# Kernel tuning notes

Measured on AMD Instinct MI355X. Metric: run time of the kernel, lower is better.

Reference implementation:

```python
import jax, jax.numpy as jnp
import numpy as np

B, L, H = 4, 96, 512
R, T = 257, 21


def setup_inputs() -> dict:
    key = jax.random.key(0)
    ks = jax.random.split(key, 7)
    std_in = (2.0 / (H + 1 + R)) ** 0.5  # xavier_normal over [H+1, R]
    return {
        "layer1": jax.random.normal(ks[0], (B, L, H), jnp.float32),
        "layer2": jax.random.normal(ks[1], (B, L, H), jnp.float32),
        "layer3": jax.random.normal(ks[2], (B, L, H), jnp.float32),
        "W_1": jax.random.normal(ks[3], (H + 1, R), jnp.float32) * std_in,
        "W_2": jax.random.normal(ks[4], (H + 1, R), jnp.float32) * std_in,
        "W_3": jax.random.normal(ks[5], (H + 1, R), jnp.float32) * std_in,
        "W_l": jax.random.normal(ks[6], (1, R, T), jnp.float32),
    }


def reference(layer1, layer2, layer3, W_1, W_2, W_3, W_l):
    # Append bias-ones feature, as in the torch forward.
    ones = jnp.ones((*layer1.shape[:2], 1), layer1.dtype)
    l1 = jnp.concatenate([layer1, ones], axis=-1)  # [n, i, H+1]
    l2 = jnp.concatenate([layer2, ones], axis=-1)  # [n, j, H+1]
    l3 = jnp.concatenate([layer3, jnp.ones((*layer3.shape[:-1], 1), layer3.dtype)], axis=-1)
    # Factor the CP contraction: project each stream to rank space first.
    p1 = jnp.einsum("nia,ar->nir", l1, W_1)  # [n, i, r]
    p2 = jnp.einsum("njb,br->njr", l2, W_2)  # [n, j, r]
    p3 = jnp.einsum("nkc,cr->nkr", l3, W_3)  # [n, k, r]
    # Fold label map into one stream, then rank-reduce outer product.
    p3t = jnp.einsum("nkr,rt->ntkr", p3, W_l[0])  # [n, t, k, r]
    out = jnp.einsum("nir,njr,ntkr->ntijk", p1, p2, p3t)  # [n, t, i, j, k]
    return out
```

## Files before the change

kernel.cpp:

```cpp
#include <hip/hip_runtime.h>
#include <hip/hip_bf16.h>

#define RR 257
#define RP 288
#define TT 21

typedef __attribute__((ext_vector_type(4))) float f32x4;
typedef __attribute__((ext_vector_type(8))) short bf16x8;

union Pack8 { unsigned short s[8]; uint4 v; };

__device__ __forceinline__ unsigned short f2b(float f) {
    union { float f; unsigned u; } v; v.f = f;
    unsigned r = v.u + 0x7fffu + ((v.u >> 16) & 1u);
    return (unsigned short)(r >> 16);
}

__global__ __launch_bounds__(384) void proj_kernel(
    const float* __restrict__ l1, const float* __restrict__ l2, const float* __restrict__ l3,
    const float* __restrict__ W1, const float* __restrict__ W2, const float* __restrict__ W3,
    float* __restrict__ P1f, float* __restrict__ P2f, float* __restrict__ P3f)
{
    int bx = blockIdx.x;
    int grp = bx % 24;
    int n = (bx / 24) & 3;
    int s = bx / 96;
    const float* layer = (s == 0) ? l1 : (s == 1) ? l2 : l3;
    const float* W     = (s == 0) ? W1 : (s == 1) ? W2 : W3;
    int i0 = grp * 4;

    __shared__ __attribute__((aligned(16))) float x[2048];
    const float4* src = (const float4*)(layer + (n * 96 + i0) * 512);
    float4* xv = (float4*)x;
    for (int idx = threadIdx.x; idx < 512; idx += 384) xv[idx] = src[idx];
    __syncthreads();

    int r = threadIdx.x;
    if (r < RP) {
        float a0 = 0.f, a1 = 0.f, a2 = 0.f, a3 = 0.f;
        if (r < RR) {
            float b = W[512 * RR + r];
            a0 = a1 = a2 = a3 = b;
            #pragma unroll 8
            for (int a = 0; a < 512; ++a) {
                float wa = W[a * RR + r];
                a0 = fmaf(x[a], wa, a0);
                a1 = fmaf(x[512 + a], wa, a1);
                a2 = fmaf(x[1024 + a], wa, a2);
                a3 = fmaf(x[1536 + a], wa, a3);
            }
        }
        float* P = (s == 0) ? P1f : (s == 1) ? P2f : P3f;
        int base = (n * 96 + i0) * RP + r;
        P[base]          = a0;
        P[base + RP]     = a1;
        P[base + 2 * RP] = a2;
        P[base + 3 * RP] = a3;
    }
}

__global__ __launch_bounds__(256) void aprep_kernel(
    const float* __restrict__ P1f, const float* __restrict__ P2f,
    unsigned short* __restrict__ Af)
{
    int bx = blockIdx.x;
    int n = bx / 96, i = bx % 96;
    __shared__ __attribute__((aligned(16))) float p1row[RP];
    for (int r = threadIdx.x; r < RP; r += 256)
        p1row[r] = P1f[(n * 96 + i) * RP + r];
    __syncthreads();

    unsigned short* dst = Af + (size_t)(n * 576 + i * 6) * 9 * 512;
    for (int idx = threadIdx.x; idx < 3456; idx += 256) {
        int L = idx & 63;
        int rest = idx >> 6;
        int ks = rest % 9, rgl = rest / 9;
        int j = rgl * 16 + (L & 15);
        int k8 = ks * 32 + (L >> 4) * 8;
        const float* p2p = P2f + (n * 96 + j) * RP + k8;
        float4 b0 = *(const float4*)(p2p);
        float4 b1 = *(const float4*)(p2p + 4);
        float4 a0 = *(const float4*)(p1row + k8);
        float4 a1 = *(const float4*)(p1row + k8 + 4);
        Pack8 u;
        u.s[0] = f2b(a0.x * b0.x); u.s[1] = f2b(a0.y * b0.y);
        u.s[2] = f2b(a0.z * b0.z); u.s[3] = f2b(a0.w * b0.w);
        u.s[4] = f2b(a1.x * b1.x); u.s[5] = f2b(a1.y * b1.y);
        u.s[6] = f2b(a1.z * b1.z); u.s[7] = f2b(a1.w * b1.w);
        *(uint4*)(dst + (size_t)(rgl * 9 + ks) * 512 + L * 8) = u.v;
    }
}

__global__ __launch_bounds__(256) void bprep_kernel(
    const float* __restrict__ P3f, const float* __restrict__ Wl,
    unsigned short* __restrict__ Bf)
{
    int bx = blockIdx.x;
    int t = bx % TT, n = bx / TT;
    __shared__ __attribute__((aligned(16))) float wl_lds[RP];
    for (int r = threadIdx.x; r < RP; r += 256)
        wl_lds[r] = (r < RR) ? Wl[r * TT + t] : 0.f;
    __syncthreads();

    unsigned short* dst = Bf + (size_t)(n * TT + t) * 6 * 9 * 512;
    for (int idx = threadIdx.x; idx < 3456; idx += 256) {
        int L = idx & 63;
        int rest = idx >> 6;
        int ks = rest % 9, kg = rest / 9;
        int col = kg * 16 + (L & 15);
        int r8 = ks * 32 + (L >> 4) * 8;
        const float* p3p = P3f + (n * 96 + col) * RP + r8;
        float4 p0 = *(const float4*)(p3p);
        float4 p1 = *(const float4*)(p3p + 4);
        float4 w0 = *(const float4*)(wl_lds + r8);
        float4 w1 = *(const float4*)(wl_lds + r8 + 4);
        Pack8 u;
        u.s[0] = f2b(p0.x * w0.x); u.s[1] = f2b(p0.y * w0.y);
        u.s[2] = f2b(p0.z * w0.z); u.s[3] = f2b(p0.w * w0.w);
        u.s[4] = f2b(p1.x * w1.x); u.s[5] = f2b(p1.y * w1.y);
        u.s[6] = f2b(p1.z * w1.z); u.s[7] = f2b(p1.w * w1.w);
        *(uint4*)(dst + (size_t)(kg * 9 + ks) * 512 + L * 8) = u.v;
    }
}

#define LOADA(s, kss) { _Pragma("unroll") for (int mf = 0; mf < 4; ++mf) \
    fa[s][mf] = *(const bf16x8*)(abase + (mf * 9 + (kss)) * 512); }
#define LOADB(s, kss) { _Pragma("unroll") for (int nf = 0; nf < 6; ++nf) \
    fb[s][nf] = *(const bf16x8*)(bbase + (nf * 9 + (kss)) * 512); }
#define MFMAS(s) { _Pragma("unroll") for (int mf = 0; mf < 4; ++mf) { \
    _Pragma("unroll") for (int nf = 0; nf < 6; ++nf) \
      acc[mf][nf] = __builtin_amdgcn_mfma_f32_16x16x32_bf16(fb[s][nf], fa[s][mf], acc[mf][nf], 0, 0, 0); } }

__global__ __launch_bounds__(256, 2) void tri4_kernel(
    const unsigned short* __restrict__ Af, const unsigned short* __restrict__ Bf,
    float* __restrict__ out)
{
    int orig = blockIdx.x;
    int bx = (orig & 7) * 378 + (orig >> 3);
    int t = bx % TT;
    int mtn = bx / TT;
    int mt = mtn % 36;
    int n = mtn / 36;

    int tid = threadIdx.x, lane = tid & 63, wv = tid >> 6;

    const unsigned short* abase = Af + (size_t)(n * 576 + mt * 16 + wv * 4) * 9 * 512 + lane * 8;
    const unsigned short* bbase = Bf + (size_t)(n * TT + t) * 6 * 9 * 512 + lane * 8;

    f32x4 acc[4][6] = {};
    bf16x8 fa[2][4], fb[2][6];

    LOADA(0, 0); LOADB(0, 0);
    #pragma unroll
    for (int kp = 0; kp < 4; ++kp) {
        LOADA(1, 2 * kp + 1); LOADB(1, 2 * kp + 1);
        MFMAS(0);
        LOADA(0, 2 * kp + 2); LOADB(0, 2 * kp + 2);
        MFMAS(1);
    }
    MFMAS(0);

    __shared__ __attribute__((aligned(16))) float tbuf[4][1600];
    int Llo = lane & 15, Lhi = lane >> 4;
    size_t outbase = ((size_t)(n * TT + t) * 9216 + mt * 256 + wv * 64) * 96;

    #pragma unroll
    for (int mf = 0; mf < 4; ++mf) {
        #pragma unroll
        for (int nf = 0; nf < 6; ++nf)
            *(f32x4*)&tbuf[wv][Llo * 100 + nf * 16 + Lhi * 4] = acc[mf][nf];
        float* gdst = out + outbase + (size_t)mf * 16 * 96;
        #pragma unroll
        for (int q = 0; q < 6; ++q) {
            int fidx = q * 64 + lane;
            int ml = fidx / 24, k4 = fidx % 24;
            f32x4 vv = *(const f32x4*)&tbuf[wv][ml * 100 + k4 * 4];
            __builtin_nontemporal_store(vv, (f32x4*)(gdst + (size_t)fidx * 4));
        }
    }
}

extern "C" void kernel_launch(void* const* d_in, const int* in_sizes, int n_in,
                              void* d_out, int out_size, void* d_ws, size_t ws_size,
                              hipStream_t stream) {
    const float* l1 = (const float*)d_in[0];
    const float* l2 = (const float*)d_in[1];
    const float* l3 = (const float*)d_in[2];
    const float* W1 = (const float*)d_in[3];
    const float* W2 = (const float*)d_in[4];
    const float* W3 = (const float*)d_in[5];
    const float* Wl = (const float*)d_in[6];

    float* P1f = (float*)d_ws;
    float* P2f = P1f + 384 * RP;
    float* P3f = P2f + 384 * RP;
    unsigned short* Af = (unsigned short*)(P3f + 384 * RP);
    unsigned short* Bf = Af + (size_t)4 * 576 * 9 * 512;

    proj_kernel<<<288, 384, 0, stream>>>(l1, l2, l3, W1, W2, W3, P1f, P2f, P3f);
    aprep_kernel<<<384, 256, 0, stream>>>(P1f, P2f, Af);
    bprep_kernel<<<84, 256, 0, stream>>>(P3f, Wl, Bf);
    tri4_kernel<<<3024, 256, 0, stream>>>(Af, Bf, (float*)d_out);
}
```

Baseline: 116.6 us.

## Stage B tile in LDS and split M across eight waves per block

The trilinear MFMA kernel now copies the per-(n,t) B operand into shared memory once per block and uses 512 threads, with each wave covering two M fragments instead of four. This removes redundant global/L2 reads of B by every wave and lowers register pressure per wave, and MFMA issue priority is raised with s_setprio. The LDS buffer is reused for the output transpose. The 55KB LDS footprint limits resident blocks per CU and adds a block-wide copy and barrier before compute.

New measurement: 121.1 us. 1.04x slower.

```diff
diff --git a/kernel.cpp b/kernel.cpp
--- a/kernel.cpp
+++ b/kernel.cpp
@@ -123,15 +123,7 @@
     }
 }
 
-#define LOADA(s, kss) { _Pragma("unroll") for (int mf = 0; mf < 4; ++mf) \
-    fa[s][mf] = *(const bf16x8*)(abase + (mf * 9 + (kss)) * 512); }
-#define LOADB(s, kss) { _Pragma("unroll") for (int nf = 0; nf < 6; ++nf) \
-    fb[s][nf] = *(const bf16x8*)(bbase + (nf * 9 + (kss)) * 512); }
-#define MFMAS(s) { _Pragma("unroll") for (int mf = 0; mf < 4; ++mf) { \
-    _Pragma("unroll") for (int nf = 0; nf < 6; ++nf) \
-      acc[mf][nf] = __builtin_amdgcn_mfma_f32_16x16x32_bf16(fb[s][nf], fa[s][mf], acc[mf][nf], 0, 0, 0); } }
-
-__global__ __launch_bounds__(256, 2) void tri4_kernel(
+__global__ __launch_bounds__(512, 4) void tri5_kernel(
     const unsigned short* __restrict__ Af, const unsigned short* __restrict__ Bf,
     float* __restrict__ out)
 {
@@ -144,37 +136,61 @@
 
     int tid = threadIdx.x, lane = tid & 63, wv = tid >> 6;
 
-    const unsigned short* abase = Af + (size_t)(n * 576 + mt * 16 + wv * 4) * 9 * 512 + lane * 8;
-    const unsigned short* bbase = Bf + (size_t)(n * TT + t) * 6 * 9 * 512 + lane * 8;
-
-    f32x4 acc[4][6] = {};
-    bf16x8 fa[2][4], fb[2][6];
-
-    LOADA(0, 0); LOADB(0, 0);
+    __shared__ __attribute__((aligned(16))) unsigned short blds[27648];
+
+    {
+        const uint4* bsrc = (const uint4*)(Bf + (size_t)(n * TT + t) * 27648);
+        uint4* bdst = (uint4*)blds;
+        for (int idx = tid; idx < 3456; idx += 512) bdst[idx] = bsrc[idx];
+    }
+    __syncthreads();
+
+    const unsigned short* abase =
+        Af + (size_t)(n * 576 + mt * 16 + wv * 2) * 9 * 512 + lane * 8;
+    const unsigned short* lbase = blds + lane * 8;
+
+    f32x4 acc[2][6] = {};
+    bf16x8 fa[2][2], fb[6];
+
+    fa[0][0] = *(const bf16x8*)(abase + 0 * 512);
+    fa[0][1] = *(const bf16x8*)(abase + 9 * 512);
+
     #pragma unroll
-    for (int kp = 0; kp < 4; ++kp) {
-        LOADA(1, 2 * kp + 1); LOADB(1, 2 * kp + 1);
-        MFMAS(0);
-        LOADA(0, 2 * kp + 2); LOADB(0, 2 * kp + 2);
-        MFMAS(1);
-    }
-    MFMAS(0);
-
-    __shared__ __attribute__((aligned(16))) float tbuf[4][1600];
+    for (int ks = 0; ks < 9; ++ks) {
+        int cur = ks & 1, nxt = cur ^ 1;
+        if (ks < 8) {
+            fa[nxt][0] = *(const bf16x8*)(abase + (0 * 9 + ks + 1) * 512);
+            fa[nxt][1] = *(const bf16x8*)(abase + (1 * 9 + ks + 1) * 512);
+        }
+        #pragma unroll
+        for (int nf = 0; nf < 6; ++nf)
+            fb[nf] = *(const bf16x8*)(lbase + (nf * 9 + ks) * 512);
+        __builtin_amdgcn_s_setprio(1);
+        #pragma unroll
+        for (int mf = 0; mf < 2; ++mf)
+            #pragma unroll
+            for (int nf = 0; nf < 6; ++nf)
+                acc[mf][nf] = __builtin_amdgcn_mfma_f32_16x16x32_bf16(
+                    fb[nf], fa[cur][mf], acc[mf][nf], 0, 0, 0);
+        __builtin_amdgcn_s_setprio(0);
+    }
+
+    __syncthreads();
+    float* tb = (float*)blds + wv * 1600;
     int Llo = lane & 15, Lhi = lane >> 4;
-    size_t outbase = ((size_t)(n * TT + t) * 9216 + mt * 256 + wv * 64) * 96;
+    size_t outbase = ((size_t)(n * TT + t) * 9216 + mt * 256 + wv * 32) * 96;
 
     #pragma unroll
-    for (int mf = 0; mf < 4; ++mf) {
+    for (int mf = 0; mf < 2; ++mf) {
         #pragma unroll
         for (int nf = 0; nf < 6; ++nf)
-            *(f32x4*)&tbuf[wv][Llo * 100 + nf * 16 + Lhi * 4] = acc[mf][nf];
+            *(f32x4*)&tb[Llo * 100 + nf * 16 + Lhi * 4] = acc[mf][nf];
         float* gdst = out + outbase + (size_t)mf * 16 * 96;
         #pragma unroll
         for (int q = 0; q < 6; ++q) {
             int fidx = q * 64 + lane;
             int ml = fidx / 24, k4 = fidx % 24;
-            f32x4 vv = *(const f32x4*)&tbuf[wv][ml * 100 + k4 * 4];
+            f32x4 vv = *(const f32x4*)&tb[ml * 100 + k4 * 4];
             __builtin_nontemporal_store(vv, (f32x4*)(gdst + (size_t)fidx * 4));
         }
     }
@@ -200,5 +216,5 @@
     proj_kernel<<<288, 384, 0, stream>>>(l1, l2, l3, W1, W2, W3, P1f, P2f, P3f);
     aprep_kernel<<<384, 256, 0, stream>>>(P1f, P2f, Af);
     bprep_kernel<<<84, 256, 0, stream>>>(P3f, Wl, Bf);
-    tri4_kernel<<<3024, 256, 0, stream>>>(Af, Bf, (float*)d_out);
-}
+    tri5_kernel<<<3024, 512, 0, stream>>>(Af, Bf, (float*)d_out);
+}
```
